# Optimization experiments

Hardware: AMD Instinct MI355X
Metric: run time of the kernel (lower is better)

## Reference

```python
import jax, jax.numpy as jnp
import numpy as np

# init kwargs baked as constants: crop_height -> depth dim, crop_length -> H, crop_width -> W
CROP_D, CROP_H, CROP_W = 16, 16, 16
EXTRAP = 0.0


def setup_inputs() -> dict:
    key = jax.random.key(0)
    k1, k2, k3 = jax.random.split(key, 3)
    N, C, D, H, W = 8, 32, 64, 64, 64
    NB = 256
    image = jax.random.normal(k1, (N, C, D, H, W), dtype=jnp.float32)
    # boxes: normalized (x1, y1, z1, x2, y2, z2) with lo <= hi per axis
    raw = jax.random.uniform(k2, (NB, 3, 2), dtype=jnp.float32)
    lo = jnp.min(raw, axis=2)
    hi = jnp.max(raw, axis=2)
    boxes = jnp.concatenate([lo, hi], axis=1)  # [NB, 6]
    box_ind = jax.random.randint(k3, (NB,), 0, N, dtype=jnp.int32)
    return {"image": image, "boxes": boxes, "box_ind": box_ind}


def _coords(lo, hi, L, c):
    # lo, hi: [nb] normalized box edges; returns [nb, c] continuous source coords
    if c > 1:
        i = jnp.arange(c, dtype=lo.dtype)
        step = (hi - lo) * (L - 1) / (c - 1)          # [nb]
        return lo[:, None] * (L - 1) + i[None, :] * step[:, None]
    return (0.5 * (lo + hi) * (L - 1))[:, None]


def _lerp_idx(coord, L):
    valid = (coord >= 0) & (coord <= L - 1)
    c = jnp.clip(coord, 0, L - 1)
    i0 = jnp.floor(c).astype(jnp.int32)
    i1 = jnp.minimum(i0 + 1, L - 1)
    frac = c - i0.astype(coord.dtype)
    return i0, i1, frac, valid


def reference(image, boxes, box_ind):
    N, C, D, H, W = image.shape
    x1, y1, z1, x2, y2, z2 = [boxes[:, k] for k in range(6)]
    zc = _coords(z1, z2, D, CROP_D)  # [nb, cd]
    yc = _coords(y1, y2, H, CROP_H)  # [nb, ch]
    xc = _coords(x1, x2, W, CROP_W)  # [nb, cw]
    z0, z1i, fz, vz = _lerp_idx(zc, D)
    y0, y1i, fy, vy = _lerp_idx(yc, H)
    x0, x1i, fx, vx = _lerp_idx(xc, W)

    img = jnp.moveaxis(image, 1, -1)  # [N, D, H, W, C] -> channels-last gather
    b = box_ind[:, None, None, None]

    def g(zi, yi, xi):
        # [nb, cd, ch, cw, C]
        return img[b, zi[:, :, None, None], yi[:, None, :, None], xi[:, None, None, :], :]

    fz_ = fz[:, :, None, None, None]
    fy_ = fy[:, None, :, None, None]
    fx_ = fx[:, None, None, :, None]

    c00 = g(z0, y0, x0) * (1 - fx_) + g(z0, y0, x1i) * fx_
    c01 = g(z0, y1i, x0) * (1 - fx_) + g(z0, y1i, x1i) * fx_
    c10 = g(z1i, y0, x0) * (1 - fx_) + g(z1i, y0, x1i) * fx_
    c11 = g(z1i, y1i, x0) * (1 - fx_) + g(z1i, y1i, x1i) * fx_
    c0 = c00 * (1 - fy_) + c01 * fy_
    c1 = c10 * (1 - fy_) + c11 * fy_
    out = c0 * (1 - fz_) + c1 * fz_  # [nb, cd, ch, cw, C]

    valid = (vz[:, :, None, None] & vy[:, None, :, None] & vx[:, None, None, :])[..., None]
    out = jnp.where(valid, out, jnp.asarray(EXTRAP, out.dtype))
    return jnp.moveaxis(out, -1, 1)  # [nb, C, cd, ch, cw]
```

## Files before the change

kernel.cpp:

```cpp
#include <hip/hip_runtime.h>
#include <stdint.h>

#define NBOX 256
#define NC   32
#define ND   64
#define NH   64
#define NW   64
#define CD   16
#define CH   16
#define CW   16
#define NXCD 8
#define DHW  (ND * NH * NW)

__global__ __launch_bounds__(NBOX) void CropAndResize3D_perm_kernel(
    const int* __restrict__ box_ind, int* __restrict__ perm)
{
    __shared__ int nsh[NBOX];
    const int t = threadIdx.x;
    nsh[t] = box_ind[t];
    __syncthreads();
    const int n_t = nsh[t];
    int rank = 0;
    #pragma unroll 8
    for (int j = 0; j < NBOX; ++j) {
        const int n_j = nsh[j];
        rank += (n_j < n_t) || (n_j == n_t && j < t);
    }
    perm[rank] = t;
}

__global__ __launch_bounds__(256) void CropAndResize3D_89481348645400_kernel(
    const float* __restrict__ image,
    const float* __restrict__ boxes,
    const int*   __restrict__ box_ind,
    const int*   __restrict__ perm,
    float*       __restrict__ out)
{
    __shared__ float sh[2 * 16 * 64];

    const int nwg_per_xcd = (NBOX * CD) / NXCD;
    const int hwid = blockIdx.x;
    const int blk = (hwid & (NXCD - 1)) * nwg_per_xcd + (hwid >> 3);

    const int slot = blk >> 4;
    const int b = perm ? perm[slot] : slot;
    const int z = blk & 15;
    const int t  = threadIdx.x;
    const int ty = t >> 4;
    const int tx = t & 15;

    const float bx1 = boxes[b*6+0], by1 = boxes[b*6+1], bz1 = boxes[b*6+2];
    const float bx2 = boxes[b*6+3], by2 = boxes[b*6+4], bz2 = boxes[b*6+5];
    const int   n   = box_ind[b];

    const float zstep = (bz2 - bz1) * 63.0f / 15.0f;
    const float ystep = (by2 - by1) * 63.0f / 15.0f;
    const float xstep = (bx2 - bx1) * 63.0f / 15.0f;

    const float zc = bz1 * 63.0f + (float)z * zstep;
    const bool  vz = (zc >= 0.0f) && (zc <= 63.0f);
    const float zq = fminf(fmaxf(zc, 0.0f), 63.0f);
    const int   z0 = (int)floorf(zq);
    const int   z1 = min(z0 + 1, ND - 1);
    const float fz = zq - (float)z0;

    const float yc = by1 * 63.0f + (float)ty * ystep;
    const bool  vy = (yc >= 0.0f) && (yc <= 63.0f);
    const float yq = fminf(fmaxf(yc, 0.0f), 63.0f);
    const int   y0 = (int)floorf(yq);
    const int   y1 = min(y0 + 1, NH - 1);
    const float fy = yq - (float)y0;

    const float xcf = bx1 * 63.0f + (float)tx * xstep;
    const bool  vx  = (xcf >= 0.0f) && (xcf <= 63.0f);
    const float xq  = fminf(fmaxf(xcf, 0.0f), 63.0f);
    const int   x0  = (int)floorf(xq);
    const int   x1  = min(x0 + 1, NW - 1);
    const float fx  = xq - (float)x0;

    const bool valid = vz && vy && vx;
    const float gz = 1.0f - fz, gy = 1.0f - fy, gx = 1.0f - fx;

    const float w00 = gz * gy, w01 = gz * fy, w10 = fz * gy, w11 = fz * fy;

    const float xcl = bx1 * 63.0f;
    const float xch = bx1 * 63.0f + 15.0f * xstep;
    const int x0min = (int)floorf(fminf(fmaxf(xcl, 0.0f), 63.0f));
    const int xlo4  = x0min & ~3;

    const int sx = min(xlo4 + (tx << 2), NW - 4);
    const int soff0 = (z0 * NH + y0) * NW + sx;
    const int soff1 = (z0 * NH + y1) * NW + sx;
    const int soff2 = (z1 * NH + y0) * NW + sx;
    const int soff3 = (z1 * NH + y1) * NW + sx;

    const int key  = (ty & 3) << 1;
    const int wadr = ty * 64 + ((tx ^ key) << 2);
    const int dx0  = x0 - xlo4;
    const int dx1  = x1 - xlo4;
    const int a0   = ty * 64 + ((((dx0 >> 2) ^ key)) << 2) + (dx0 & 3);
    const int a1   = ty * 64 + ((((dx1 >> 2) ^ key)) << 2) + (dx1 & 3);

    const float* imgb = image + (size_t)n * (NC * DHW);
    float* op = out + (size_t)b * (NC * CD * CH * CW) + (z * CH + ty) * CW + tx;

    float4 A0, A1, A2, A3, B0, B1, B2, B3;

    #define ISSUE(Ra, Rb, Rc, Rd, c)  do {                                     \
        const float* p_ = imgb + (size_t)(c) * DHW;                            \
        Ra = *(const float4*)(p_ + soff0);                                     \
        Rb = *(const float4*)(p_ + soff1);                                     \
        Rc = *(const float4*)(p_ + soff2);                                     \
        Rd = *(const float4*)(p_ + soff3);                                     \
    } while (0)

    #define CWRITE(Ra, Rb, Rc, Rd, c)  do {                                    \
        float4 o_;                                                             \
        o_.x = Ra.x * w00 + Rb.x * w01 + Rc.x * w10 + Rd.x * w11;              \
        o_.y = Ra.y * w00 + Rb.y * w01 + Rc.y * w10 + Rd.y * w11;              \
        o_.z = Ra.z * w00 + Rb.z * w01 + Rc.z * w10 + Rd.z * w11;              \
        o_.w = Ra.w * w00 + Rb.w * w01 + Rc.w * w10 + Rd.w * w11;              \
        *(float4*)(sh + (((c) & 1) << 10) + wadr) = o_;                        \
    } while (0)

    #define COMPUTE(c)  do {                                                   \
        const float* S_ = sh + (((c) & 1) << 10);                              \
        const float s0 = S_[a0], s1 = S_[a1];                                  \
        float v = s0 * gx + s1 * fx;                                           \
        v = valid ? v : 0.0f;                                                  \
        __builtin_nontemporal_store(v, op + (c) * (CD * CH * CW));             \
    } while (0)

    ISSUE(A0, A1, A2, A3, 0);
    CWRITE(A0, A1, A2, A3, 0);
    ISSUE(B0, B1, B2, B3, 1);

    #pragma unroll
    for (int c = 0; c < NC; c += 2) {
        if (c + 2 < NC) ISSUE(A0, A1, A2, A3, c + 2);
        COMPUTE(c);
        if (c + 1 < NC) CWRITE(B0, B1, B2, B3, c + 1);
        __builtin_amdgcn_s_barrier();
        if (c + 1 < NC) {
            if (c + 3 < NC) ISSUE(B0, B1, B2, B3, c + 3);
            COMPUTE(c + 1);
            if (c + 2 < NC) CWRITE(A0, A1, A2, A3, c + 2);
            __builtin_amdgcn_s_barrier();
        }
    }

    #undef ISSUE
    #undef CWRITE
    #undef COMPUTE
}

extern "C" void kernel_launch(void* const* d_in, const int* in_sizes, int n_in,
                              void* d_out, int out_size, void* d_ws, size_t ws_size,
                              hipStream_t stream) {
    const float* image   = (const float*)d_in[0];
    const float* boxes   = (const float*)d_in[1];
    const int*   box_ind = (const int*)d_in[2];
    float*       out     = (float*)d_out;

    int* perm = nullptr;
    if (ws_size >= NBOX * sizeof(int)) {
        perm = (int*)d_ws;
        CropAndResize3D_perm_kernel<<<1, NBOX, 0, stream>>>(box_ind, perm);
    }

    const int blocks = NBOX * CD;
    CropAndResize3D_89481348645400_kernel<<<blocks, 256, 0, stream>>>(
        image, boxes, box_ind, perm, out);
}
```

Measured before the change: 129.2 us.

## Deepen channel prefetch to four stages and skip loads for idle lanes

The channel loop moves from double buffering to four register sets, so loads for channels c+4..c+7 are in flight while channel c is blended. The shared-memory write and the x-interpolation read now happen back to back in each step, with one barrier per channel. Lanes whose 4-wide x segment lies outside the box's x span no longer issue global loads, which cuts redundant memory requests. This costs more vector registers, which may lower occupancy, and it depends on LDS write-then-read ordering within a wavefront for correctness.

```diff
diff --git a/kernel.cpp b/kernel.cpp
--- a/kernel.cpp
+++ b/kernel.cpp
@@ -86,7 +86,11 @@
     const float xcl = bx1 * 63.0f;
     const float xch = bx1 * 63.0f + 15.0f * xstep;
     const int x0min = (int)floorf(fminf(fmaxf(xcl, 0.0f), 63.0f));
+    const int x1max = min((int)floorf(fminf(fmaxf(xch, 0.0f), 63.0f)) + 1, NW - 1);
     const int xlo4  = x0min & ~3;
+    const int G     = ((x1max - xlo4) >> 2) + 1;
+
+    const bool act = (tx < G);
 
     const int sx = min(xlo4 + (tx << 2), NW - 4);
     const int soff0 = (z0 * NH + y0) * NW + sx;
@@ -104,15 +108,17 @@
     const float* imgb = image + (size_t)n * (NC * DHW);
     float* op = out + (size_t)b * (NC * CD * CH * CW) + (z * CH + ty) * CW + tx;
 
-    float4 A0, A1, A2, A3, B0, B1, B2, B3;
+    float4 A0 = {0,0,0,0}, A1 = {0,0,0,0}, A2 = {0,0,0,0}, A3 = {0,0,0,0};
+    float4 B0 = {0,0,0,0}, B1 = {0,0,0,0}, B2 = {0,0,0,0}, B3 = {0,0,0,0};
+    float4 C0 = {0,0,0,0}, C1 = {0,0,0,0}, C2 = {0,0,0,0}, C3 = {0,0,0,0};
+    float4 D0 = {0,0,0,0}, D1 = {0,0,0,0}, D2 = {0,0,0,0}, D3 = {0,0,0,0};
 
-    #define ISSUE(Ra, Rb, Rc, Rd, c)  do {                                     \
+    #define ISSUE(Ra, Rb, Rc, Rd, c)  do { if (act) {                          \
         const float* p_ = imgb + (size_t)(c) * DHW;                            \
         Ra = *(const float4*)(p_ + soff0);                                     \
         Rb = *(const float4*)(p_ + soff1);                                     \
         Rc = *(const float4*)(p_ + soff2);                                     \
-        Rd = *(const float4*)(p_ + soff3);                                     \
-    } while (0)
+        Rd = *(const float4*)(p_ + soff3); } } while (0)
 
     #define CWRITE(Ra, Rb, Rc, Rd, c)  do {                                    \
         float4 o_;                                                             \
@@ -132,21 +138,27 @@
     } while (0)
 
     ISSUE(A0, A1, A2, A3, 0);
-    CWRITE(A0, A1, A2, A3, 0);
     ISSUE(B0, B1, B2, B3, 1);
+    ISSUE(C0, C1, C2, C3, 2);
+    ISSUE(D0, D1, D2, D3, 3);
 
     #pragma unroll
-    for (int c = 0; c < NC; c += 2) {
-        if (c + 2 < NC) ISSUE(A0, A1, A2, A3, c + 2);
-        COMPUTE(c);
-        if (c + 1 < NC) CWRITE(B0, B1, B2, B3, c + 1);
+    for (int c = 0; c < NC; c += 4) {
+        CWRITE(A0, A1, A2, A3, c    );  COMPUTE(c    );
+        if (c + 4 < NC) ISSUE(A0, A1, A2, A3, c + 4);
         __builtin_amdgcn_s_barrier();
-        if (c + 1 < NC) {
-            if (c + 3 < NC) ISSUE(B0, B1, B2, B3, c + 3);
-            COMPUTE(c + 1);
-            if (c + 2 < NC) CWRITE(A0, A1, A2, A3, c + 2);
-            __builtin_amdgcn_s_barrier();
-        }
+
+        CWRITE(B0, B1, B2, B3, c + 1);  COMPUTE(c + 1);
+        if (c + 5 < NC) ISSUE(B0, B1, B2, B3, c + 5);
+        __builtin_amdgcn_s_barrier();
+
+        CWRITE(C0, C1, C2, C3, c + 2);  COMPUTE(c + 2);
+        if (c + 6 < NC) ISSUE(C0, C1, C2, C3, c + 6);
+        __builtin_amdgcn_s_barrier();
+
+        CWRITE(D0, D1, D2, D3, c + 3);  COMPUTE(c + 3);
+        if (c + 7 < NC) ISSUE(D0, D1, D2, D3, c + 7);
+        __builtin_amdgcn_s_barrier();
     }
 
     #undef ISSUE
```

After: 113.6 us. -12.1%, faster.
